# Performance work log

Hardware: AMD Instinct MI355X
Metric: run time of the kernel (lower is better)

Reference implementation:

```python
import jax, jax.numpy as jnp
import numpy as np

N = 50000      # nodes
E = 800000     # edges (avg degree 16)
D_IN = 64
D_H = 64
D_OUT = 64


def setup_inputs() -> dict:
    key = jax.random.key(0)
    ks = jax.random.split(key, 8)
    x = jax.random.normal(ks[0], (N, D_IN), dtype=jnp.float32)
    edge_index = jax.random.randint(ks[1], (2, E), 0, N, dtype=jnp.int32)
    s1 = 1.0 / np.sqrt(D_IN)
    s2 = 1.0 / np.sqrt(D_H)
    s3 = 1.0 / np.sqrt(D_OUT)
    W1 = jax.random.uniform(ks[2], (D_IN, D_H), jnp.float32, -s1, s1)
    b1 = jnp.zeros((D_H,), jnp.float32)
    W2 = jax.random.uniform(ks[3], (D_H, D_OUT), jnp.float32, -s2, s2)
    b2 = jnp.zeros((D_OUT,), jnp.float32)
    Wfc = jax.random.uniform(ks[4], (D_OUT, 1), jnp.float32, -s3, s3)
    bfc = jax.random.uniform(ks[5], (1,), jnp.float32, -s3, s3)
    return {"x": x, "edge_index": edge_index, "W1": W1, "b1": b1,
            "W2": W2, "b2": b2, "Wfc": Wfc, "bfc": bfc}


def gcn_conv(x, W, b, src, dst, norm, n):
    """PyG GCNConv: h = x@W; out_i = sum_{(s,i)} norm * h_s ; + bias."""
    h = x @ W                                     # [N, d_out]
    msg = h[src] * norm[:, None]                  # [E+N, d_out] gather
    agg = jax.ops.segment_sum(msg, dst, num_segments=n)  # scatter-add
    return agg + b


def reference(x, edge_index, W1, b1, W2, b2, Wfc, bfc):
    n = x.shape[0]
    # add self-loops (PyG default add_self_loops=True)
    loops = jnp.arange(n, dtype=edge_index.dtype)
    src = jnp.concatenate([edge_index[0], loops])
    dst = jnp.concatenate([edge_index[1], loops])
    # symmetric normalization deg^{-1/2} (deg computed with self-loops, >=1)
    deg = jnp.zeros((n,), x.dtype).at[dst].add(1.0)
    dinv = jax.lax.rsqrt(deg)
    norm = dinv[src] * dinv[dst]                  # [E+N]
    h = jax.nn.relu(gcn_conv(x, W1, b1, src, dst, norm, n))
    # dropout is identity in eval mode
    h = jax.nn.relu(gcn_conv(h, W2, b2, src, dst, norm, n))
    out = h @ Wfc + bfc                           # [N, 1]
    out = jnp.mean(out, axis=0, keepdims=True)    # [1, 1]
    return jax.nn.sigmoid(out)
```

## Files before the change

### kernel.cpp

```cpp
#include <hip/hip_runtime.h>
#include <hip/hip_fp16.h>
#include <math.h>

#define N_NODES 50000
#define N_EDGES 800000
#define D_FEAT 64

#define NBUCKET 196
#define PART_BLOCKS 196
#define PART_EPB 4096
#define BCAP 6144

#define GEMM_BLOCKS (N_NODES / 16)
#define AGG_BLOCKS 1568
#define N_PAD (NBUCKET * 256)


__global__ __launch_bounds__(256) void k_zero(int* __restrict__ gcount) {
    if (threadIdx.x < NBUCKET) gcount[threadIdx.x] = 0;
}

__global__ __launch_bounds__(256) void k_part(const int* __restrict__ src,
                                              const int* __restrict__ dst,
                                              int* __restrict__ gcount,
                                              unsigned* __restrict__ ebuf) {
    __shared__ unsigned eloc[PART_EPB];
    __shared__ int cnt[NBUCKET];
    int tid = threadIdx.x;
    for (int i = tid; i < NBUCKET; i += 256) cnt[i] = 0;
    __syncthreads();
    int e0 = blockIdx.x * PART_EPB;
    int n = N_EDGES - e0; if (n > PART_EPB) n = PART_EPB;
    for (int k = tid; k < n; k += 256) {
        int e = e0 + k;
        int d = dst[e];
        eloc[k] = (unsigned)src[e] | ((unsigned)(d & 255) << 16) | ((unsigned)(d >> 8) << 24);
        atomicAdd(&cnt[d >> 8], 1);
    }
    __syncthreads();
    for (int i = tid; i < NBUCKET; i += 256)
        cnt[i] = atomicAdd(&gcount[i], cnt[i]);
    __syncthreads();
    for (int k = tid; k < n; k += 256) {
        unsigned p = eloc[k];
        int b = p >> 24;
        int slot = atomicAdd(&cnt[b], 1);
        if (slot < BCAP) ebuf[(size_t)b * BCAP + slot] = p;
    }
}

__global__ __launch_bounds__(256) void k_p2group(const unsigned* __restrict__ ebuf,
                                                 const int* __restrict__ gcount,
                                                 int* __restrict__ rowbeg,
                                                 int* __restrict__ rowdeg,
                                                 ushort* __restrict__ colsrc,
                                                 float* __restrict__ dinv) {
    __shared__ unsigned eloc[BCAP];
    __shared__ int hist[256];
    __shared__ int sh[256];
    int tid = threadIdx.x;
    int b = blockIdx.x;
    int cnt = gcount[b]; if (cnt > BCAP) cnt = BCAP;
    hist[tid] = 0;
    __syncthreads();
    for (int i = tid; i < cnt; i += 256) {
        unsigned p = ebuf[(size_t)b * BCAP + i];
        eloc[i] = p;
        atomicAdd(&hist[(p >> 16) & 255], 1);
    }
    __syncthreads();
    int v = hist[tid];
    sh[tid] = v;
    __syncthreads();
    #pragma unroll
    for (int off = 1; off < 256; off <<= 1) {
        int t = (tid >= off) ? sh[tid - off] : 0;
        __syncthreads();
        sh[tid] += t;
        __syncthreads();
    }
    int binoff = sh[tid] - v;
    int node = b * 256 + tid;
    rowbeg[node] = b * BCAP + binoff;
    rowdeg[node] = v;
    dinv[node] = rsqrtf((float)(v + 1));
    hist[tid] = binoff;
    __syncthreads();
    for (int i = tid; i < cnt; i += 256) {
        unsigned p = eloc[i];
        int slot = b * BCAP + atomicAdd(&hist[(p >> 16) & 255], 1);
        colsrc[slot] = (ushort)(p & 0xFFFFu);
    }
}


__global__ __launch_bounds__(256) void k_gemm_f32(const float* __restrict__ X,
                                                  const float* __restrict__ W,
                                                  const float* __restrict__ dinv,
                                                  __half* __restrict__ out) {
    __shared__ float Wl[64][64];
    int tid = threadIdx.x;
    {
        const float4* Wv = (const float4*)W;
        float4* Wlv = (float4*)&Wl[0][0];
        #pragma unroll
        for (int i = 0; i < 4; ++i) Wlv[tid + 256 * i] = Wv[tid + 256 * i];
    }
    __syncthreads();
    int r = blockIdx.x * 16 + (tid >> 4);
    int c0 = (tid & 15) << 2;
    const float4* xrow = (const float4*)(X + (size_t)r * D_FEAT);
    float ax = 0.f, ay = 0.f, az = 0.f, aw = 0.f;
    #pragma unroll
    for (int k4 = 0; k4 < 16; ++k4) {
        float4 xv = xrow[k4];
        #pragma unroll
        for (int j = 0; j < 4; ++j) {
            float xs = (j == 0) ? xv.x : (j == 1) ? xv.y : (j == 2) ? xv.z : xv.w;
            const float4 wv = *(const float4*)&Wl[4 * k4 + j][c0];
            ax += xs * wv.x; ay += xs * wv.y; az += xs * wv.z; aw += xs * wv.w;
        }
    }
    float sc = dinv[r];
    union { __half2 h2[2]; uint2 u2; } cvt;
    cvt.h2[0] = __floats2half2_rn(ax * sc, ay * sc);
    cvt.h2[1] = __floats2half2_rn(az * sc, aw * sc);
    *(uint2*)(out + (size_t)r * D_FEAT + c0) = cvt.u2;
}

__global__ __launch_bounds__(256) void k_gemm_f16(const __half* __restrict__ X,
                                                  const float* __restrict__ W,
                                                  const float* __restrict__ dinv,
                                                  __half* __restrict__ out) {
    __shared__ float Wl[64][64];
    int tid = threadIdx.x;
    {
        const float4* Wv = (const float4*)W;
        float4* Wlv = (float4*)&Wl[0][0];
        #pragma unroll
        for (int i = 0; i < 4; ++i) Wlv[tid + 256 * i] = Wv[tid + 256 * i];
    }
    __syncthreads();
    int r = blockIdx.x * 16 + (tid >> 4);
    int c0 = (tid & 15) << 2;
    const __half2* xrow = (const __half2*)(X + (size_t)r * D_FEAT);
    float ax = 0.f, ay = 0.f, az = 0.f, aw = 0.f;
    #pragma unroll
    for (int k4 = 0; k4 < 16; ++k4) {
        float2 lo = __half22float2(xrow[2 * k4]);
        float2 hi = __half22float2(xrow[2 * k4 + 1]);
        #pragma unroll
        for (int j = 0; j < 4; ++j) {
            float xs = (j == 0) ? lo.x : (j == 1) ? lo.y : (j == 2) ? hi.x : hi.y;
            const float4 wv = *(const float4*)&Wl[4 * k4 + j][c0];
            ax += xs * wv.x; ay += xs * wv.y; az += xs * wv.z; aw += xs * wv.w;
        }
    }
    float sc = dinv[r];
    union { __half2 h2[2]; uint2 u2; } cvt;
    cvt.h2[0] = __floats2half2_rn(ax * sc, ay * sc);
    cvt.h2[1] = __floats2half2_rn(az * sc, aw * sc);
    *(uint2*)(out + (size_t)r * D_FEAT + c0) = cvt.u2;
}


__device__ __forceinline__ void addh8(float acc[8], uint4 r) {
    union { uint4 u; __half2 h[4]; } c; c.u = r;
    #pragma unroll
    for (int i = 0; i < 4; ++i) {
        float2 f = __half22float2(c.h[i]);
        acc[2 * i]     += f.x;
        acc[2 * i + 1] += f.y;
    }
}

__device__ __forceinline__ void agg_core(const __half* __restrict__ hm,
                                         const ushort* __restrict__ colsrc,
                                         int beg, int deg, int o, float acc[8]) {
    const uint4* hv = (const uint4*)hm;
    int j = 0;
    for (; j + 4 <= deg; j += 4) {
        int s0 = colsrc[beg + j];
        int s1 = colsrc[beg + j + 1];
        int s2 = colsrc[beg + j + 2];
        int s3 = colsrc[beg + j + 3];
        uint4 r0 = hv[(size_t)s0 * 8 + o];
        uint4 r1 = hv[(size_t)s1 * 8 + o];
        uint4 r2 = hv[(size_t)s2 * 8 + o];
        uint4 r3 = hv[(size_t)s3 * 8 + o];
        addh8(acc, r0); addh8(acc, r1); addh8(acc, r2); addh8(acc, r3);
    }
    for (; j < deg; ++j) {
        int s = colsrc[beg + j];
        addh8(acc, hv[(size_t)s * 8 + o]);
    }
}

__global__ __launch_bounds__(256) void k_agg_relu(const __half* __restrict__ hm,
                                                  const int* __restrict__ rowbeg,
                                                  const int* __restrict__ rowdeg,
                                                  const ushort* __restrict__ colsrc,
                                                  const float* __restrict__ dinv,
                                                  const float* __restrict__ bias,
                                                  __half* __restrict__ outp) {
    int lane = threadIdx.x & 63;
    int wid = threadIdx.x >> 6;
    int node = (blockIdx.x * 4 + wid) * 8 + (lane >> 3);
    int o = lane & 7;
    bool valid = node < N_NODES;
    float acc[8];
    #pragma unroll
    for (int i = 0; i < 8; ++i) acc[i] = 0.f;
    if (valid) {
        const uint4* hv = (const uint4*)hm;
        addh8(acc, hv[(size_t)node * 8 + o]);
        agg_core(hm, colsrc, rowbeg[node], rowdeg[node], o, acc);
        float di = dinv[node];
        const float4* b4 = (const float4*)bias;
        float4 bl = b4[o * 2], bh = b4[o * 2 + 1];
        union { uint4 u; __half2 h[4]; } st;
        st.h[0] = __floats2half2_rn(fmaxf(di * acc[0] + bl.x, 0.f), fmaxf(di * acc[1] + bl.y, 0.f));
        st.h[1] = __floats2half2_rn(fmaxf(di * acc[2] + bl.z, 0.f), fmaxf(di * acc[3] + bl.w, 0.f));
        st.h[2] = __floats2half2_rn(fmaxf(di * acc[4] + bh.x, 0.f), fmaxf(di * acc[5] + bh.y, 0.f));
        st.h[3] = __floats2half2_rn(fmaxf(di * acc[6] + bh.z, 0.f), fmaxf(di * acc[7] + bh.w, 0.f));
        *(uint4*)(outp + (size_t)node * D_FEAT + o * 8) = st.u;
    }
}

__global__ __launch_bounds__(256) void k_agg2_dot(const __half* __restrict__ hm,
                                                  const int* __restrict__ rowbeg,
                                                  const int* __restrict__ rowdeg,
                                                  const ushort* __restrict__ colsrc,
                                                  const float* __restrict__ dinv,
                                                  const float* __restrict__ bias,
                                                  const float* __restrict__ Wfc,
                                                  float* __restrict__ partials) {
    __shared__ float red[4];
    int lane = threadIdx.x & 63;
    int wid = threadIdx.x >> 6;
    int node = (blockIdx.x * 4 + wid) * 8 + (lane >> 3);
    int o = lane & 7;
    bool valid = node < N_NODES;
    float acc[8];
    #pragma unroll
    for (int i = 0; i < 8; ++i) acc[i] = 0.f;
    float s = 0.f;
    if (valid) {
        const uint4* hv = (const uint4*)hm;
        addh8(acc, hv[(size_t)node * 8 + o]);
        agg_core(hm, colsrc, rowbeg[node], rowdeg[node], o, acc);
        float di = dinv[node];
        const float4* b4 = (const float4*)bias;
        const float4* w4 = (const float4*)Wfc;
        float4 bl = b4[o * 2], bh = b4[o * 2 + 1];
        float4 wl = w4[o * 2], wh = w4[o * 2 + 1];
        s  = fmaxf(di * acc[0] + bl.x, 0.f) * wl.x;
        s += fmaxf(di * acc[1] + bl.y, 0.f) * wl.y;
        s += fmaxf(di * acc[2] + bl.z, 0.f) * wl.z;
        s += fmaxf(di * acc[3] + bl.w, 0.f) * wl.w;
        s += fmaxf(di * acc[4] + bh.x, 0.f) * wh.x;
        s += fmaxf(di * acc[5] + bh.y, 0.f) * wh.y;
        s += fmaxf(di * acc[6] + bh.z, 0.f) * wh.z;
        s += fmaxf(di * acc[7] + bh.w, 0.f) * wh.w;
    }
    #pragma unroll
    for (int m = 1; m < 64; m <<= 1) s += __shfl_xor(s, m, 64);
    if (lane == 0) red[wid] = s;
    __syncthreads();
    if (threadIdx.x == 0) partials[blockIdx.x] = red[0] + red[1] + red[2] + red[3];
}

__global__ __launch_bounds__(256) void k_final(const float* __restrict__ partials,
                                               const float* __restrict__ bfc,
                                               float* __restrict__ out) {
    __shared__ float red[4];
    float s = 0.0f;
    for (int i = threadIdx.x; i < AGG_BLOCKS; i += 256) s += partials[i];
    #pragma unroll
    for (int off = 32; off > 0; off >>= 1) s += __shfl_down(s, off, 64);
    if ((threadIdx.x & 63) == 0) red[threadIdx.x >> 6] = s;
    __syncthreads();
    if (threadIdx.x == 0) {
        float t = red[0] + red[1] + red[2] + red[3];
        float z = t / (float)N_NODES + bfc[0];
        out[0] = 1.0f / (1.0f + expf(-z));
    }
}


extern "C" void kernel_launch(void* const* d_in, const int* in_sizes, int n_in,
                              void* d_out, int out_size, void* d_ws, size_t ws_size,
                              hipStream_t stream) {
    const float* x   = (const float*)d_in[0];
    const int*   ei  = (const int*)d_in[1];
    const int*   src = ei;
    const int*   dst = ei + N_EDGES;
    const float* W1  = (const float*)d_in[2];
    const float* b1  = (const float*)d_in[3];
    const float* W2  = (const float*)d_in[4];
    const float* b2  = (const float*)d_in[5];
    const float* Wfc = (const float*)d_in[6];
    const float* bfc = (const float*)d_in[7];
    float* out = (float*)d_out;

    char* ws = (char*)d_ws;
    size_t off = 0;
    auto alloc = [&](size_t bytes) -> char* {
        char* p = ws + off;
        off += (bytes + 255) & ~(size_t)255;
        return p;
    };
    int*      gcount   = (int*)alloc((size_t)NBUCKET * 4);
    unsigned* ebuf     = (unsigned*)alloc((size_t)NBUCKET * BCAP * 4);
    ushort*   colsrc   = (ushort*)alloc((size_t)NBUCKET * BCAP * 2);
    int*      rowbeg   = (int*)alloc((size_t)N_PAD * 4);
    int*      rowdeg   = (int*)alloc((size_t)N_PAD * 4);
    float*    dinv     = (float*)alloc((size_t)N_PAD * 4);
    float*    partials = (float*)alloc((size_t)AGG_BLOCKS * 4);
    __half*   bufA     = (__half*)alloc((size_t)N_NODES * D_FEAT * 2);
    __half*   bufB     = (__half*)alloc((size_t)N_NODES * D_FEAT * 2);

    k_zero     <<<1,           256, 0, stream>>>(gcount);
    k_part     <<<PART_BLOCKS, 256, 0, stream>>>(src, dst, gcount, ebuf);
    k_p2group  <<<NBUCKET,     256, 0, stream>>>(ebuf, gcount, rowbeg, rowdeg, colsrc, dinv);

    k_gemm_f32 <<<GEMM_BLOCKS, 256, 0, stream>>>(x, W1, dinv, bufA);
    k_agg_relu <<<AGG_BLOCKS,  256, 0, stream>>>(bufA, rowbeg, rowdeg, colsrc, dinv, b1, bufB);

    k_gemm_f16 <<<GEMM_BLOCKS, 256, 0, stream>>>(bufB, W2, dinv, bufA);
    k_agg2_dot <<<AGG_BLOCKS,  256, 0, stream>>>(bufA, rowbeg, rowdeg, colsrc, dinv, b2, Wfc, partials);

    k_final    <<<1, 256, 0, stream>>>(partials, bfc, out);
}
```

Measured before the change: 93.31 us.

## Fuse layer-2 GEMM into layer-1 aggregation and deepen gather unrolling

Layer 1's aggregation kernel now also computes relu(agg)@W2 scaled by dinv. Each 8-lane group shuffles its node's hidden row among its lanes and multiplies against W2 staged in shared memory. This drops the separate f16 GEMM launch and one full write and read of the N x 64 half-precision intermediate. The neighbor gather loop is also unrolled to 8 outstanding loads for more memory-level parallelism. The cost is more shuffles, more LDS reads and more registers in the aggregation kernel, which may lower occupancy.

```diff
diff --git a/kernel.cpp b/kernel.cpp
--- a/kernel.cpp
+++ b/kernel.cpp
@@ -128,41 +128,6 @@
     *(uint2*)(out + (size_t)r * D_FEAT + c0) = cvt.u2;
 }
 
-__global__ __launch_bounds__(256) void k_gemm_f16(const __half* __restrict__ X,
-                                                  const float* __restrict__ W,
-                                                  const float* __restrict__ dinv,
-                                                  __half* __restrict__ out) {
-    __shared__ float Wl[64][64];
-    int tid = threadIdx.x;
-    {
-        const float4* Wv = (const float4*)W;
-        float4* Wlv = (float4*)&Wl[0][0];
-        #pragma unroll
-        for (int i = 0; i < 4; ++i) Wlv[tid + 256 * i] = Wv[tid + 256 * i];
-    }
-    __syncthreads();
-    int r = blockIdx.x * 16 + (tid >> 4);
-    int c0 = (tid & 15) << 2;
-    const __half2* xrow = (const __half2*)(X + (size_t)r * D_FEAT);
-    float ax = 0.f, ay = 0.f, az = 0.f, aw = 0.f;
-    #pragma unroll
-    for (int k4 = 0; k4 < 16; ++k4) {
-        float2 lo = __half22float2(xrow[2 * k4]);
-        float2 hi = __half22float2(xrow[2 * k4 + 1]);
-        #pragma unroll
-        for (int j = 0; j < 4; ++j) {
-            float xs = (j == 0) ? lo.x : (j == 1) ? lo.y : (j == 2) ? hi.x : hi.y;
-            const float4 wv = *(const float4*)&Wl[4 * k4 + j][c0];
-            ax += xs * wv.x; ay += xs * wv.y; az += xs * wv.z; aw += xs * wv.w;
-        }
-    }
-    float sc = dinv[r];
-    union { __half2 h2[2]; uint2 u2; } cvt;
-    cvt.h2[0] = __floats2half2_rn(ax * sc, ay * sc);
-    cvt.h2[1] = __floats2half2_rn(az * sc, aw * sc);
-    *(uint2*)(out + (size_t)r * D_FEAT + c0) = cvt.u2;
-}
-
 
 __device__ __forceinline__ void addh8(float acc[8], uint4 r) {
     union { uint4 u; __half2 h[4]; } c; c.u = r;
@@ -179,16 +144,24 @@
                                          int beg, int deg, int o, float acc[8]) {
     const uint4* hv = (const uint4*)hm;
     int j = 0;
-    for (; j + 4 <= deg; j += 4) {
-        int s0 = colsrc[beg + j];
-        int s1 = colsrc[beg + j + 1];
-        int s2 = colsrc[beg + j + 2];
-        int s3 = colsrc[beg + j + 3];
-        uint4 r0 = hv[(size_t)s0 * 8 + o];
-        uint4 r1 = hv[(size_t)s1 * 8 + o];
-        uint4 r2 = hv[(size_t)s2 * 8 + o];
-        uint4 r3 = hv[(size_t)s3 * 8 + o];
-        addh8(acc, r0); addh8(acc, r1); addh8(acc, r2); addh8(acc, r3);
+    for (; j + 8 <= deg; j += 8) {
+        int s[8]; uint4 r[8];
+        #pragma unroll
+        for (int u = 0; u < 8; ++u) s[u] = colsrc[beg + j + u];
+        #pragma unroll
+        for (int u = 0; u < 8; ++u) r[u] = hv[(size_t)s[u] * 8 + o];
+        #pragma unroll
+        for (int u = 0; u < 8; ++u) addh8(acc, r[u]);
+    }
+    if (j + 4 <= deg) {
+        int s[4]; uint4 r[4];
+        #pragma unroll
+        for (int u = 0; u < 4; ++u) s[u] = colsrc[beg + j + u];
+        #pragma unroll
+        for (int u = 0; u < 4; ++u) r[u] = hv[(size_t)s[u] * 8 + o];
+        #pragma unroll
+        for (int u = 0; u < 4; ++u) addh8(acc, r[u]);
+        j += 4;
     }
     for (; j < deg; ++j) {
         int s = colsrc[beg + j];
@@ -196,36 +169,73 @@
     }
 }
 
-__global__ __launch_bounds__(256) void k_agg_relu(const __half* __restrict__ hm,
-                                                  const int* __restrict__ rowbeg,
-                                                  const int* __restrict__ rowdeg,
-                                                  const ushort* __restrict__ colsrc,
-                                                  const float* __restrict__ dinv,
-                                                  const float* __restrict__ bias,
-                                                  __half* __restrict__ outp) {
+
+__global__ __launch_bounds__(256) void k_agg1_g2(const __half* __restrict__ hm,
+                                                 const int* __restrict__ rowbeg,
+                                                 const int* __restrict__ rowdeg,
+                                                 const ushort* __restrict__ colsrc,
+                                                 const float* __restrict__ dinv,
+                                                 const float* __restrict__ b1,
+                                                 const float* __restrict__ W2,
+                                                 __half* __restrict__ outp) {
+    __shared__ float Wl[64][64];
+    {
+        const float4* Wv = (const float4*)W2;
+        float4* Wlv = (float4*)&Wl[0][0];
+        #pragma unroll
+        for (int i = 0; i < 4; ++i) Wlv[threadIdx.x + 256 * i] = Wv[threadIdx.x + 256 * i];
+    }
+    __syncthreads();
     int lane = threadIdx.x & 63;
     int wid = threadIdx.x >> 6;
     int node = (blockIdx.x * 4 + wid) * 8 + (lane >> 3);
     int o = lane & 7;
     bool valid = node < N_NODES;
-    float acc[8];
-    #pragma unroll
-    for (int i = 0; i < 8; ++i) acc[i] = 0.f;
     if (valid) {
+        float acc[8];
+        #pragma unroll
+        for (int i = 0; i < 8; ++i) acc[i] = 0.f;
         const uint4* hv = (const uint4*)hm;
         addh8(acc, hv[(size_t)node * 8 + o]);
         agg_core(hm, colsrc, rowbeg[node], rowdeg[node], o, acc);
         float di = dinv[node];
-        const float4* b4 = (const float4*)bias;
+        const float4* b4 = (const float4*)b1;
         float4 bl = b4[o * 2], bh = b4[o * 2 + 1];
+        float h1[8];
+        h1[0] = fmaxf(di * acc[0] + bl.x, 0.f);
+        h1[1] = fmaxf(di * acc[1] + bl.y, 0.f);
+        h1[2] = fmaxf(di * acc[2] + bl.z, 0.f);
+        h1[3] = fmaxf(di * acc[3] + bl.w, 0.f);
+        h1[4] = fmaxf(di * acc[4] + bh.x, 0.f);
+        h1[5] = fmaxf(di * acc[5] + bh.y, 0.f);
+        h1[6] = fmaxf(di * acc[6] + bh.z, 0.f);
+        h1[7] = fmaxf(di * acc[7] + bh.w, 0.f);
+        float oa[8];
+        #pragma unroll
+        for (int i = 0; i < 8; ++i) oa[i] = 0.f;
+        int gbase = lane & 56;
+        #pragma unroll
+        for (int g = 0; g < 8; ++g) {
+            #pragma unroll
+            for (int j = 0; j < 8; ++j) {
+                float hk = __shfl(h1[j], gbase | g, 64);
+                const float4 w0 = *(const float4*)&Wl[g * 8 + j][o * 8];
+                const float4 w1 = *(const float4*)&Wl[g * 8 + j][o * 8 + 4];
+                oa[0] += hk * w0.x; oa[1] += hk * w0.y;
+                oa[2] += hk * w0.z; oa[3] += hk * w0.w;
+                oa[4] += hk * w1.x; oa[5] += hk * w1.y;
+                oa[6] += hk * w1.z; oa[7] += hk * w1.w;
+            }
+        }
         union { uint4 u; __half2 h[4]; } st;
-        st.h[0] = __floats2half2_rn(fmaxf(di * acc[0] + bl.x, 0.f), fmaxf(di * acc[1] + bl.y, 0.f));
-        st.h[1] = __floats2half2_rn(fmaxf(di * acc[2] + bl.z, 0.f), fmaxf(di * acc[3] + bl.w, 0.f));
-        st.h[2] = __floats2half2_rn(fmaxf(di * acc[4] + bh.x, 0.f), fmaxf(di * acc[5] + bh.y, 0.f));
-        st.h[3] = __floats2half2_rn(fmaxf(di * acc[6] + bh.z, 0.f), fmaxf(di * acc[7] + bh.w, 0.f));
+        st.h[0] = __floats2half2_rn(oa[0] * di, oa[1] * di);
+        st.h[1] = __floats2half2_rn(oa[2] * di, oa[3] * di);
+        st.h[2] = __floats2half2_rn(oa[4] * di, oa[5] * di);
+        st.h[3] = __floats2half2_rn(oa[6] * di, oa[7] * di);
         *(uint4*)(outp + (size_t)node * D_FEAT + o * 8) = st.u;
     }
 }
+
 
 __global__ __launch_bounds__(256) void k_agg2_dot(const __half* __restrict__ hm,
                                                   const int* __restrict__ rowbeg,
@@ -241,11 +251,11 @@
     int node = (blockIdx.x * 4 + wid) * 8 + (lane >> 3);
     int o = lane & 7;
     bool valid = node < N_NODES;
-    float acc[8];
-    #pragma unroll
-    for (int i = 0; i < 8; ++i) acc[i] = 0.f;
     float s = 0.f;
     if (valid) {
+        float acc[8];
+        #pragma unroll
+        for (int i = 0; i < 8; ++i) acc[i] = 0.f;
         const uint4* hv = (const uint4*)hm;
         addh8(acc, hv[(size_t)node * 8 + o]);
         agg_core(hm, colsrc, rowbeg[node], rowdeg[node], o, acc);
@@ -325,10 +335,10 @@
     k_p2group  <<<NBUCKET,     256, 0, stream>>>(ebuf, gcount, rowbeg, rowdeg, colsrc, dinv);
 
     k_gemm_f32 <<<GEMM_BLOCKS, 256, 0, stream>>>(x, W1, dinv, bufA);
-    k_agg_relu <<<AGG_BLOCKS,  256, 0, stream>>>(bufA, rowbeg, rowdeg, colsrc, dinv, b1, bufB);
-
-    k_gemm_f16 <<<GEMM_BLOCKS, 256, 0, stream>>>(bufB, W2, dinv, bufA);
-    k_agg2_dot <<<AGG_BLOCKS,  256, 0, stream>>>(bufA, rowbeg, rowdeg, colsrc, dinv, b2, Wfc, partials);
+
+    k_agg1_g2  <<<AGG_BLOCKS,  256, 0, stream>>>(bufA, rowbeg, rowdeg, colsrc, dinv, b1, W2, bufB);
+
+    k_agg2_dot <<<AGG_BLOCKS,  256, 0, stream>>>(bufB, rowbeg, rowdeg, colsrc, dinv, b2, Wfc, partials);
 
     k_final    <<<1, 256, 0, stream>>>(partials, bfc, out);
 }
```

New measurement: 88.64 us. 1.05x faster.
